# Optimization experiments

Hardware: AMD Instinct MI355X
Metric: run time of the kernel (lower is better)

Reference implementation:

```python
import jax, jax.numpy as jnp
import numpy as np

B, N, D, C = 64, 512, 1024, 4  # batch, num_electrodes, d_model, num_classes
H = D // 2


def setup_inputs() -> dict:
    key = jax.random.key(0)
    ks = jax.random.split(key, 16)
    s = 0.02
    return {
        "Q": jax.random.normal(ks[0], (B, N, D), jnp.float32),
        "K": jax.random.normal(ks[1], (B, N, D), jnp.float32),
        "V": jax.random.normal(ks[2], (B, N, D), jnp.float32),
        "electrode_ids": jnp.arange(N, dtype=jnp.int64 if jax.config.jax_enable_x64 else jnp.int32),
        "emb": jax.random.normal(ks[3], (N, D), jnp.float32) * s,
        "dw1": jax.random.normal(ks[4], (H, D), jnp.float32) * s,
        "db1": jnp.zeros((H,), jnp.float32),
        "dw2": jax.random.normal(ks[5], (1, H), jnp.float32) * s,
        "db2": jnp.zeros((1,), jnp.float32),
        "sw1": jax.random.normal(ks[6], (H, D), jnp.float32) * s,
        "sb1": jnp.zeros((H,), jnp.float32),
        "sw2": jax.random.normal(ks[7], (1, H), jnp.float32) * s,
        "sb2": jnp.zeros((1,), jnp.float32),
        "dopamine_scale": jnp.asarray(1.0, jnp.float32),
        "serotonin_scale": jnp.asarray(1.0, jnp.float32),
        "fc_w": jax.random.normal(ks[8], (C, N * D), jnp.float32) * s,
        "fc_b": jnp.zeros((C,), jnp.float32),
    }


def reference(Q, K, V, electrode_ids, emb, dw1, db1, dw2, db2,
              sw1, sb1, sw2, sb2, dopamine_scale, serotonin_scale, fc_w, fc_b):
    e = emb[electrode_ids]                       # [N, D]
    Q = Q + e
    K = K + e
    V = V + e
    scale = jnp.sqrt(jnp.asarray(D, jnp.float32))
    scores = jnp.einsum('bnd,bmd->bnm', Q, K) / scale          # [B, N, N]
    probs = jax.nn.softmax(scores, axis=-1)
    entropy = -jnp.sum(probs * jnp.log(probs + 1e-6), axis=-1)  # [B, N]

    # dopamine MLP on Q tokens (eval mode -> dropout is identity)
    dh = jax.nn.relu(jnp.einsum('bnd,hd->bnh', Q, dw1) + db1)
    dopamine = jax.nn.sigmoid(jnp.einsum('bnh,oh->bno', dh, dw2) + db2)[..., 0]  # [B, N]

    # serotonin MLP on entropy broadcast to D identical features:
    # Linear(entropy * ones(D)) == entropy * W1.sum(axis=1) + b1 (same math, no [B,N,D] temp)
    sh = jax.nn.relu(entropy[..., None] * jnp.sum(sw1, axis=1) + sb1)            # [B, N, H]
    serotonin = jax.nn.sigmoid(jnp.einsum('bnh,oh->bno', sh, sw2) + sb2)[..., 0]  # [B, N]

    mod = dopamine_scale * dopamine[..., None] - serotonin_scale * serotonin[..., None]
    ms = scores + mod
    mu = jnp.mean(ms, axis=-1, keepdims=True)
    sd = jnp.std(ms, axis=-1, keepdims=True, ddof=1)  # torch.std default is unbiased
    ms = (ms - mu) / (sd + 1e-6)
    probs2 = jax.nn.softmax(ms, axis=-1)
    attn_out = jnp.einsum('bnm,bmd->bnd', probs2, V)   # [B, N, D]
    flat = attn_out.reshape(attn_out.shape[0], -1)      # [B, N*D]
    return flat @ fc_w.T + fc_b                          # [B, C]
```

## Files before the change

kernel.cpp:

```cpp
#include <hip/hip_runtime.h>

#define NN 512
#define ND 1024
#define NDW 524288
#define NBATCH 64

typedef __attribute__((ext_vector_type(8))) __bf16 bf16x8;
typedef __attribute__((ext_vector_type(4))) float f32x4;
typedef unsigned short u16;
typedef unsigned int u32;

__device__ __forceinline__ u16 f2bf(float x) {
    u32 u = __float_as_uint(x);
    u = (u + 0x7fffu + ((u >> 16) & 1u)) >> 16;
    return (u16)u;
}
__device__ __forceinline__ float bf2f(u16 x) {
    return __uint_as_float(((u32)x) << 16);
}

union BF8 { bf16x8 v; u16 s[8]; };

__device__ __forceinline__ void dma16(const u16* g, const u16* l) {
    __builtin_amdgcn_global_load_lds(
        (const __attribute__((address_space(1))) u32*)(uintptr_t)g,
        (__attribute__((address_space(3))) u32*)(u32)(uintptr_t)l,
        16, 0, 0);
}

__global__ __launch_bounds__(256)
void nma_init_out(float* __restrict__ out, const float* __restrict__ fcb) {
    int t = threadIdx.x;
    if (t < NBATCH * 4) out[t] = fcb[t & 3];
}

__global__ __launch_bounds__(256)
void prep_ke(const float* __restrict__ K, const int* __restrict__ eid,
             const float* __restrict__ emb, u16* __restrict__ Ke) {
    size_t f = ((size_t)blockIdx.x * 256 + threadIdx.x) * 8;
    int n = (int)((f >> 10) & (NN - 1));
    int col = (int)(f & (ND - 1));
    const float* kp = K + f;
    const float* ep = emb + (size_t)eid[n] * ND + col;
    float4 k0 = *(const float4*)kp, k1 = *(const float4*)(kp + 4);
    float4 e0 = *(const float4*)ep, e1 = *(const float4*)(ep + 4);
    union { uint4 q; u16 s[8]; } o;
    o.s[0]=f2bf(k0.x+e0.x); o.s[1]=f2bf(k0.y+e0.y); o.s[2]=f2bf(k0.z+e0.z); o.s[3]=f2bf(k0.w+e0.w);
    o.s[4]=f2bf(k1.x+e1.x); o.s[5]=f2bf(k1.y+e1.y); o.s[6]=f2bf(k1.z+e1.z); o.s[7]=f2bf(k1.w+e1.w);
    *(uint4*)(Ke + f) = o.q;
}

__global__ __launch_bounds__(256)
void prep_vt(const float* __restrict__ V, const int* __restrict__ eid,
             const float* __restrict__ emb, u16* __restrict__ VT) {
    __shared__ u16 T[64 * 72];
    const int tid = threadIdx.x;
    const int b = blockIdx.z, d0 = blockIdx.y * 64, n0 = blockIdx.x * 64;
    {
        const int r = tid >> 2, cs = (tid & 3) * 16;
        const int n = n0 + r;
        const float* vp = V + ((size_t)b * NN + n) * ND + d0 + cs;
        const float* ep = emb + (size_t)eid[n] * ND + d0 + cs;
        #pragma unroll
        for (int j = 0; j < 4; ++j) {
            float4 v = *(const float4*)(vp + j * 4);
            float4 e = *(const float4*)(ep + j * 4);
            T[(cs + j*4 + 0) * 72 + r] = f2bf(v.x + e.x);
            T[(cs + j*4 + 1) * 72 + r] = f2bf(v.y + e.y);
            T[(cs + j*4 + 2) * 72 + r] = f2bf(v.z + e.z);
            T[(cs + j*4 + 3) * 72 + r] = f2bf(v.w + e.w);
        }
    }
    __syncthreads();
    {
        const int dr = tid >> 2, ms = (tid & 3) * 16;
        u16* dst = VT + ((size_t)b * ND + d0 + dr) * NN + n0 + ms;
        *(uint4*)dst       = *(const uint4*)&T[dr * 72 + ms];
        *(uint4*)(dst + 8) = *(const uint4*)&T[dr * 72 + ms + 8];
    }
}

__global__ __launch_bounds__(256, 2)
void nma_attn(const float* __restrict__ Q, const int* __restrict__ eid,
              const float* __restrict__ emb, const u16* __restrict__ Ke,
              const u16* __restrict__ VT, u16* __restrict__ O)
{
    __shared__ __align__(16) u16 KV[NN * 32];
    __shared__ __align__(16) u16 Ps[32 * 520];
    __shared__ float red[4][32][4];
    __shared__ float rowM[32], rowInv[32], rowRden[32];

    const int tid  = threadIdx.x;
    const int w    = tid >> 6;
    const int lane = tid & 63;
    const int q    = lane >> 4;
    const int l15  = lane & 15;
    const int bid  = blockIdx.x;
    const int jj   = bid >> 3;
    const int b    = (bid & 7) + ((jj >> 4) << 3);
    const int i0   = (jj & 15) * 32;
    const size_t bOff = (size_t)b * NN * ND;

    const float* Qrow0 = Q + bOff + (size_t)(i0 + l15) * ND;
    const float* Qrow1 = Q + bOff + (size_t)(i0 + 16 + l15) * ND;
    const float* Erow0 = emb + (size_t)eid[i0 + l15] * ND;
    const float* Erow1 = emb + (size_t)eid[i0 + 16 + l15] * ND;

    const u16* KeB = Ke + bOff;
    const u16* VTB = VT + (size_t)b * ND * NN;
    const int liw = w * 64 + lane;

    f32x4 acc[2][8];
    #pragma unroll
    for (int it = 0; it < 2; ++it)
        #pragma unroll
        for (int mt = 0; mt < 8; ++mt)
            acc[it][mt] = (f32x4){0.f, 0.f, 0.f, 0.f};

    for (int kc = 0; kc < 32; ++kc) {
        __syncthreads();
        #pragma unroll
        for (int ii = 0; ii < 8; ++ii) {
            const int li = ii * 256 + liw;
            const int m = li >> 2, seg = li & 3;
            dma16(KeB + (size_t)m * ND + kc * 32 + seg * 8,
                  &KV[(size_t)(ii * 256 + w * 64) * 8]);
        }
        BF8 a0u, a1u;
        {
            const int k0 = kc * 32 + q * 8;
            float4 x0 = *(const float4*)(Qrow0 + k0);
            float4 x1 = *(const float4*)(Qrow0 + k0 + 4);
            float4 e0 = *(const float4*)(Erow0 + k0);
            float4 e1 = *(const float4*)(Erow0 + k0 + 4);
            a0u.s[0] = f2bf(x0.x + e0.x); a0u.s[1] = f2bf(x0.y + e0.y);
            a0u.s[2] = f2bf(x0.z + e0.z); a0u.s[3] = f2bf(x0.w + e0.w);
            a0u.s[4] = f2bf(x1.x + e1.x); a0u.s[5] = f2bf(x1.y + e1.y);
            a0u.s[6] = f2bf(x1.z + e1.z); a0u.s[7] = f2bf(x1.w + e1.w);
            x0 = *(const float4*)(Qrow1 + k0);
            x1 = *(const float4*)(Qrow1 + k0 + 4);
            e0 = *(const float4*)(Erow1 + k0);
            e1 = *(const float4*)(Erow1 + k0 + 4);
            a1u.s[0] = f2bf(x0.x + e0.x); a1u.s[1] = f2bf(x0.y + e0.y);
            a1u.s[2] = f2bf(x0.z + e0.z); a1u.s[3] = f2bf(x0.w + e0.w);
            a1u.s[4] = f2bf(x1.x + e1.x); a1u.s[5] = f2bf(x1.y + e1.y);
            a1u.s[6] = f2bf(x1.z + e1.z); a1u.s[7] = f2bf(x1.w + e1.w);
        }
        __syncthreads();
        #pragma unroll
        for (int mt = 0; mt < 8; ++mt) {
            bf16x8 bf = *(const bf16x8*)&KV[(w * 128 + mt * 16 + l15) * 32 + q * 8];
            acc[0][mt] = __builtin_amdgcn_mfma_f32_16x16x32_bf16(a0u.v, bf, acc[0][mt], 0, 0, 0);
            acc[1][mt] = __builtin_amdgcn_mfma_f32_16x16x32_bf16(a1u.v, bf, acc[1][mt], 0, 0, 0);
        }
    }

    const float SC = 0.03125f;
    #pragma unroll
    for (int it = 0; it < 2; ++it)
        #pragma unroll
        for (int mt = 0; mt < 8; ++mt) {
            acc[it][mt][0] *= SC; acc[it][mt][1] *= SC;
            acc[it][mt][2] *= SC; acc[it][mt][3] *= SC;
        }
    float ssum[2][4], ssq[2][4], smax[2][4];
    #pragma unroll
    for (int it = 0; it < 2; ++it)
        #pragma unroll
        for (int r = 0; r < 4; ++r) {
            float s = 0.f, s2 = 0.f, mx = -3.4e38f;
            #pragma unroll
            for (int mt = 0; mt < 8; ++mt) {
                float v = acc[it][mt][r];
                s += v; s2 += v * v; mx = fmaxf(mx, v);
            }
            #pragma unroll
            for (int d = 1; d < 16; d <<= 1) {
                s  += __shfl_xor(s, d);
                s2 += __shfl_xor(s2, d);
                mx  = fmaxf(mx, __shfl_xor(mx, d));
            }
            ssum[it][r] = s; ssq[it][r] = s2; smax[it][r] = mx;
        }
    if (l15 == 0) {
        #pragma unroll
        for (int it = 0; it < 2; ++it)
            #pragma unroll
            for (int r = 0; r < 4; ++r) {
                int i = it * 16 + q * 4 + r;
                red[w][i][0] = ssum[it][r];
                red[w][i][1] = ssq[it][r];
                red[w][i][2] = smax[it][r];
            }
    }
    __syncthreads();
    if (tid < 32) {
        float s  = red[0][tid][0] + red[1][tid][0] + red[2][tid][0] + red[3][tid][0];
        float s2 = red[0][tid][1] + red[1][tid][1] + red[2][tid][1] + red[3][tid][1];
        float mx = fmaxf(fmaxf(red[0][tid][2], red[1][tid][2]),
                         fmaxf(red[2][tid][2], red[3][tid][2]));
        float mu  = s * (1.f / 512.f);
        float var = fmaxf((s2 - s * mu) * (1.f / 511.f), 0.f);
        float sd  = sqrtf(var);
        rowM[tid]   = mx;
        rowInv[tid] = 1.f / (sd + 1e-6f);
    }
    __syncthreads();
    float dsum[2][4];
    #pragma unroll
    for (int it = 0; it < 2; ++it)
        #pragma unroll
        for (int r = 0; r < 4; ++r) {
            int i = it * 16 + q * 4 + r;
            float M = rowM[i], inv = rowInv[i];
            float s = 0.f;
            #pragma unroll
            for (int mt = 0; mt < 8; ++mt) {
                float e = __expf((acc[it][mt][r] - M) * inv);
                acc[it][mt][r] = e; s += e;
            }
            #pragma unroll
            for (int d = 1; d < 16; d <<= 1) s += __shfl_xor(s, d);
            dsum[it][r] = s;
        }
    if (l15 == 0) {
        #pragma unroll
        for (int it = 0; it < 2; ++it)
            #pragma unroll
            for (int r = 0; r < 4; ++r)
                red[w][it * 16 + q * 4 + r][0] = dsum[it][r];
    }
    __syncthreads();
    if (tid < 32)
        rowRden[tid] = 1.f / (red[0][tid][0] + red[1][tid][0] + red[2][tid][0] + red[3][tid][0]);
    __syncthreads();
    #pragma unroll
    for (int it = 0; it < 2; ++it)
        #pragma unroll
        for (int r = 0; r < 4; ++r) {
            int i = it * 16 + q * 4 + r;
            float rd = rowRden[i];
            #pragma unroll
            for (int mt = 0; mt < 8; ++mt) {
                int m = w * 128 + mt * 16 + l15;
                Ps[i * 520 + m] = f2bf(acc[it][mt][r] * rd);
            }
        }

    for (int h = 0; h < 2; ++h) {
        f32x4 oacc[2][8];
        #pragma unroll
        for (int it = 0; it < 2; ++it)
            #pragma unroll
            for (int dt = 0; dt < 8; ++dt)
                oacc[it][dt] = (f32x4){0.f, 0.f, 0.f, 0.f};
        for (int mc = 0; mc < 16; ++mc) {
            __syncthreads();
            #pragma unroll
            for (int ii = 0; ii < 8; ++ii) {
                const int li = ii * 256 + liw;
                const int r = li >> 2, seg = li & 3;
                dma16(VTB + (size_t)(h * 512 + r) * NN + mc * 32 + seg * 8,
                      &KV[(size_t)(ii * 256 + w * 64) * 8]);
            }
            __syncthreads();
            bf16x8 p0 = *(const bf16x8*)&Ps[l15 * 520 + mc * 32 + q * 8];
            bf16x8 p1 = *(const bf16x8*)&Ps[(16 + l15) * 520 + mc * 32 + q * 8];
            #pragma unroll
            for (int dt = 0; dt < 8; ++dt) {
                bf16x8 bf = *(const bf16x8*)&KV[(w * 128 + dt * 16 + l15) * 32 + q * 8];
                oacc[0][dt] = __builtin_amdgcn_mfma_f32_16x16x32_bf16(p0, bf, oacc[0][dt], 0, 0, 0);
                oacc[1][dt] = __builtin_amdgcn_mfma_f32_16x16x32_bf16(p1, bf, oacc[1][dt], 0, 0, 0);
            }
        }
        #pragma unroll
        for (int it = 0; it < 2; ++it)
            #pragma unroll
            for (int dt = 0; dt < 8; ++dt) {
                const int dglob = h * 512 + w * 128 + dt * 16 + l15;
                #pragma unroll
                for (int r = 0; r < 4; ++r) {
                    const int iglob = i0 + it * 16 + q * 4 + r;
                    O[bOff + (size_t)iglob * ND + dglob] = f2bf(oacc[it][dt][r]);
                }
            }
    }
}

__global__ __launch_bounds__(256)
void fc_red(const u16* __restrict__ O, const float* __restrict__ fcw,
            float* __restrict__ out)
{
    __shared__ __align__(16) u16 Osh[64 * 264];
    __shared__ __align__(16) float Fsh[4 * 260];
    const int tid = threadIdx.x;
    const size_t nbase = (size_t)blockIdx.x * 1024;
    const int b = tid >> 2, c = tid & 3;
    float sum = 0.f;
    for (int ch = 0; ch < 4; ++ch) {
        __syncthreads();
        #pragma unroll
        for (int ii = 0; ii < 8; ++ii) {
            int si = ii * 256 + tid;
            int row = si >> 5, col8 = (si & 31) * 8;
            *(uint4*)&Osh[row * 264 + col8] =
                *(const uint4*)(O + (size_t)row * NDW + nbase + ch * 256 + col8);
        }
        {
            int cc = tid >> 6, n4 = (tid & 63) * 4;
            *(float4*)&Fsh[cc * 260 + n4] =
                *(const float4*)(fcw + (size_t)cc * NDW + nbase + ch * 256 + n4);
        }
        __syncthreads();
        #pragma unroll 4
        for (int n8 = 0; n8 < 32; ++n8) {
            union { uint4 v; u16 s[8]; } o4;
            o4.v = *(const uint4*)&Osh[b * 264 + n8 * 8];
            float4 f0 = *(const float4*)&Fsh[c * 260 + n8 * 8];
            float4 f1 = *(const float4*)&Fsh[c * 260 + n8 * 8 + 4];
            sum += bf2f(o4.s[0]) * f0.x + bf2f(o4.s[1]) * f0.y
                 + bf2f(o4.s[2]) * f0.z + bf2f(o4.s[3]) * f0.w
                 + bf2f(o4.s[4]) * f1.x + bf2f(o4.s[5]) * f1.y
                 + bf2f(o4.s[6]) * f1.z + bf2f(o4.s[7]) * f1.w;
        }
    }
    atomicAdd(&out[b * 4 + c], sum);
}

extern "C" void kernel_launch(void* const* d_in, const int* in_sizes, int n_in,
                              void* d_out, int out_size, void* d_ws, size_t ws_size,
                              hipStream_t stream) {
    (void)in_sizes; (void)n_in; (void)ws_size; (void)out_size;
    const float* Q   = (const float*)d_in[0];
    const float* K   = (const float*)d_in[1];
    const float* V   = (const float*)d_in[2];
    const int*   eid = (const int*)d_in[3];
    const float* emb = (const float*)d_in[4];
    const float* fcw = (const float*)d_in[15];
    const float* fcb = (const float*)d_in[16];
    float* out = (float*)d_out;

    u16* Ke = (u16*)d_ws;
    u16* VT = Ke + (size_t)NBATCH * NN * ND;
    u16* O  = VT + (size_t)NBATCH * NN * ND;

    nma_init_out<<<dim3(1), dim3(256), 0, stream>>>(out, fcb);
    prep_ke<<<dim3(16384), dim3(256), 0, stream>>>(K, eid, emb, Ke);
    prep_vt<<<dim3(8, 16, 64), dim3(256), 0, stream>>>(V, eid, emb, VT);
    nma_attn<<<dim3(1024), dim3(256), 0, stream>>>(Q, eid, emb, Ke, VT, O);
    fc_red<<<dim3(512), dim3(256), 0, stream>>>(O, fcw, out);
}
```

Measured before the change: 743.1 us.

## Make K/V tile DMA wave-private and software-pipeline loads to drop block barriers

The K and V^T tile DMA into LDS is remapped so each wave loads only the 128 rows it consumes itself. That removes the need for the two __syncthreads per k-chunk; explicit vmcnt/lgkmcnt waits are used instead. The next chunk's DMA is issued right after the current LDS fragments are read into registers, and the Q+emb global loads are double-buffered in registers. This overlaps memory traffic with MFMA work, at the cost of more registers and reliance on hand-tuned waitcnt ordering with global_load_lds.

```diff
diff --git a/kernel.cpp b/kernel.cpp
--- a/kernel.cpp
+++ b/kernel.cpp
@@ -95,20 +95,37 @@
     const int lane = tid & 63;
     const int q    = lane >> 4;
     const int l15  = lane & 15;
+    const int rr   = lane >> 2;
+    const int seg  = lane & 3;
     const int bid  = blockIdx.x;
     const int jj   = bid >> 3;
     const int b    = (bid & 7) + ((jj >> 4) << 3);
     const int i0   = (jj & 15) * 32;
     const size_t bOff = (size_t)b * NN * ND;
-
-    const float* Qrow0 = Q + bOff + (size_t)(i0 + l15) * ND;
-    const float* Qrow1 = Q + bOff + (size_t)(i0 + 16 + l15) * ND;
-    const float* Erow0 = emb + (size_t)eid[i0 + l15] * ND;
-    const float* Erow1 = emb + (size_t)eid[i0 + 16 + l15] * ND;
+    const int wrow = w * 128;
+
+    const float* Qr0 = Q + bOff + (size_t)(i0 + l15) * ND;
+    const float* Qr1 = Q + bOff + (size_t)(i0 + 16 + l15) * ND;
+    const float* Er0 = emb + (size_t)eid[i0 + l15] * ND;
+    const float* Er1 = emb + (size_t)eid[i0 + 16 + l15] * ND;
 
     const u16* KeB = Ke + bOff;
     const u16* VTB = VT + (size_t)b * ND * NN;
-    const int liw = w * 64 + lane;
+
+#define DMA_KE(KC) do {                                                         \
+    _Pragma("unroll")                                                           \
+    for (int ii_ = 0; ii_ < 8; ++ii_)                                           \
+        dma16(KeB + (size_t)(wrow + ii_ * 16 + rr) * ND + (KC) * 32 + seg * 8,  \
+              &KV[(wrow + ii_ * 16) * 32]);                                     \
+    } while (0)
+
+#define DMA_VT(H, MC) do {                                                      \
+    _Pragma("unroll")                                                           \
+    for (int ii_ = 0; ii_ < 8; ++ii_)                                           \
+        dma16(VTB + (size_t)((H) * 512 + wrow + ii_ * 16 + rr) * NN             \
+                  + (MC) * 32 + seg * 8,                                        \
+              &KV[(wrow + ii_ * 16) * 32]);                                     \
+    } while (0)
 
     f32x4 acc[2][8];
     #pragma unroll
@@ -117,42 +134,51 @@
         for (int mt = 0; mt < 8; ++mt)
             acc[it][mt] = (f32x4){0.f, 0.f, 0.f, 0.f};
 
-    for (int kc = 0; kc < 32; ++kc) {
-        __syncthreads();
-        #pragma unroll
-        for (int ii = 0; ii < 8; ++ii) {
-            const int li = ii * 256 + liw;
-            const int m = li >> 2, seg = li & 3;
-            dma16(KeB + (size_t)m * ND + kc * 32 + seg * 8,
-                  &KV[(size_t)(ii * 256 + w * 64) * 8]);
-        }
-        BF8 a0u, a1u;
-        {
-            const int k0 = kc * 32 + q * 8;
-            float4 x0 = *(const float4*)(Qrow0 + k0);
-            float4 x1 = *(const float4*)(Qrow0 + k0 + 4);
-            float4 e0 = *(const float4*)(Erow0 + k0);
-            float4 e1 = *(const float4*)(Erow0 + k0 + 4);
-            a0u.s[0] = f2bf(x0.x + e0.x); a0u.s[1] = f2bf(x0.y + e0.y);
-            a0u.s[2] = f2bf(x0.z + e0.z); a0u.s[3] = f2bf(x0.w + e0.w);
-            a0u.s[4] = f2bf(x1.x + e1.x); a0u.s[5] = f2bf(x1.y + e1.y);
-            a0u.s[6] = f2bf(x1.z + e1.z); a0u.s[7] = f2bf(x1.w + e1.w);
-            x0 = *(const float4*)(Qrow1 + k0);
-            x1 = *(const float4*)(Qrow1 + k0 + 4);
-            e0 = *(const float4*)(Erow1 + k0);
-            e1 = *(const float4*)(Erow1 + k0 + 4);
-            a1u.s[0] = f2bf(x0.x + e0.x); a1u.s[1] = f2bf(x0.y + e0.y);
-            a1u.s[2] = f2bf(x0.z + e0.z); a1u.s[3] = f2bf(x0.w + e0.w);
-            a1u.s[4] = f2bf(x1.x + e1.x); a1u.s[5] = f2bf(x1.y + e1.y);
-            a1u.s[6] = f2bf(x1.z + e1.z); a1u.s[7] = f2bf(x1.w + e1.w);
-        }
-        __syncthreads();
-        #pragma unroll
-        for (int mt = 0; mt < 8; ++mt) {
-            bf16x8 bf = *(const bf16x8*)&KV[(w * 128 + mt * 16 + l15) * 32 + q * 8];
-            acc[0][mt] = __builtin_amdgcn_mfma_f32_16x16x32_bf16(a0u.v, bf, acc[0][mt], 0, 0, 0);
-            acc[1][mt] = __builtin_amdgcn_mfma_f32_16x16x32_bf16(a1u.v, bf, acc[1][mt], 0, 0, 0);
-        }
+    float4 cur[8], nxt[8];
+    {
+        const int k0 = q * 8;
+        cur[0] = *(const float4*)(Qr0 + k0); cur[1] = *(const float4*)(Qr0 + k0 + 4);
+        cur[2] = *(const float4*)(Er0 + k0); cur[3] = *(const float4*)(Er0 + k0 + 4);
+        cur[4] = *(const float4*)(Qr1 + k0); cur[5] = *(const float4*)(Qr1 + k0 + 4);
+        cur[6] = *(const float4*)(Er1 + k0); cur[7] = *(const float4*)(Er1 + k0 + 4);
+        DMA_KE(0);
+    }
+
+#define P2BODY(KC, CUR, NXT) do {                                               \
+    BF8 a0u, a1u;                                                               \
+    a0u.s[0]=f2bf(CUR[0].x+CUR[2].x); a0u.s[1]=f2bf(CUR[0].y+CUR[2].y);         \
+    a0u.s[2]=f2bf(CUR[0].z+CUR[2].z); a0u.s[3]=f2bf(CUR[0].w+CUR[2].w);         \
+    a0u.s[4]=f2bf(CUR[1].x+CUR[3].x); a0u.s[5]=f2bf(CUR[1].y+CUR[3].y);         \
+    a0u.s[6]=f2bf(CUR[1].z+CUR[3].z); a0u.s[7]=f2bf(CUR[1].w+CUR[3].w);         \
+    a1u.s[0]=f2bf(CUR[4].x+CUR[6].x); a1u.s[1]=f2bf(CUR[4].y+CUR[6].y);         \
+    a1u.s[2]=f2bf(CUR[4].z+CUR[6].z); a1u.s[3]=f2bf(CUR[4].w+CUR[6].w);         \
+    a1u.s[4]=f2bf(CUR[5].x+CUR[7].x); a1u.s[5]=f2bf(CUR[5].y+CUR[7].y);         \
+    a1u.s[6]=f2bf(CUR[5].z+CUR[7].z); a1u.s[7]=f2bf(CUR[5].w+CUR[7].w);         \
+    if ((KC) < 31) {                                                            \
+        const int k0 = ((KC) + 1) * 32 + q * 8;                                 \
+        NXT[0] = *(const float4*)(Qr0 + k0); NXT[1] = *(const float4*)(Qr0 + k0 + 4); \
+        NXT[2] = *(const float4*)(Er0 + k0); NXT[3] = *(const float4*)(Er0 + k0 + 4); \
+        NXT[4] = *(const float4*)(Qr1 + k0); NXT[5] = *(const float4*)(Qr1 + k0 + 4); \
+        NXT[6] = *(const float4*)(Er1 + k0); NXT[7] = *(const float4*)(Er1 + k0 + 4); \
+        asm volatile("s_waitcnt vmcnt(8)" ::: "memory");      \
+    } else {                                                                    \
+        asm volatile("s_waitcnt vmcnt(0)" ::: "memory");                        \
+    }                                                                           \
+    bf16x8 bfr[8];                                                              \
+    _Pragma("unroll")                                                           \
+    for (int mt = 0; mt < 8; ++mt)                                              \
+        bfr[mt] = *(const bf16x8*)&KV[(wrow + mt * 16 + l15) * 32 + q * 8];     \
+    asm volatile("s_waitcnt lgkmcnt(0)" ::: "memory");          \
+    if ((KC) < 31) DMA_KE((KC) + 1);                     \
+    _Pragma("unroll")                                                           \
+    for (int mt = 0; mt < 8; ++mt) {                                            \
+        acc[0][mt] = __builtin_amdgcn_mfma_f32_16x16x32_bf16(a0u.v, bfr[mt], acc[0][mt], 0, 0, 0); \
+        acc[1][mt] = __builtin_amdgcn_mfma_f32_16x16x32_bf16(a1u.v, bfr[mt], acc[1][mt], 0, 0, 0); \
+    } } while (0)
+
+    for (int kc = 0; kc < 32; kc += 2) {
+        P2BODY(kc, cur, nxt);
+        P2BODY(kc + 1, nxt, cur);
     }
 
     const float SC = 0.03125f;
@@ -246,7 +272,9 @@
                 Ps[i * 520 + m] = f2bf(acc[it][mt][r] * rd);
             }
         }
-
+    __syncthreads();
+
+    DMA_VT(0, 0);
     for (int h = 0; h < 2; ++h) {
         f32x4 oacc[2][8];
         #pragma unroll
@@ -255,22 +283,23 @@
             for (int dt = 0; dt < 8; ++dt)
                 oacc[it][dt] = (f32x4){0.f, 0.f, 0.f, 0.f};
         for (int mc = 0; mc < 16; ++mc) {
-            __syncthreads();
-            #pragma unroll
-            for (int ii = 0; ii < 8; ++ii) {
-                const int li = ii * 256 + liw;
-                const int r = li >> 2, seg = li & 3;
-                dma16(VTB + (size_t)(h * 512 + r) * NN + mc * 32 + seg * 8,
-                      &KV[(size_t)(ii * 256 + w * 64) * 8]);
-            }
-            __syncthreads();
             bf16x8 p0 = *(const bf16x8*)&Ps[l15 * 520 + mc * 32 + q * 8];
             bf16x8 p1 = *(const bf16x8*)&Ps[(16 + l15) * 520 + mc * 32 + q * 8];
+            asm volatile("s_waitcnt vmcnt(0)" ::: "memory");
+            bf16x8 bfr[8];
+            #pragma unroll
+            for (int dt = 0; dt < 8; ++dt)
+                bfr[dt] = *(const bf16x8*)&KV[(wrow + dt * 16 + l15) * 32 + q * 8];
+            asm volatile("s_waitcnt lgkmcnt(0)" ::: "memory");
+            const int j = h * 16 + mc;
+            if (j < 31) {
+                const int jn = j + 1;
+                DMA_VT(jn >> 4, jn & 15);
+            }
             #pragma unroll
             for (int dt = 0; dt < 8; ++dt) {
-                bf16x8 bf = *(const bf16x8*)&KV[(w * 128 + dt * 16 + l15) * 32 + q * 8];
-                oacc[0][dt] = __builtin_amdgcn_mfma_f32_16x16x32_bf16(p0, bf, oacc[0][dt], 0, 0, 0);
-                oacc[1][dt] = __builtin_amdgcn_mfma_f32_16x16x32_bf16(p1, bf, oacc[1][dt], 0, 0, 0);
+                oacc[0][dt] = __builtin_amdgcn_mfma_f32_16x16x32_bf16(p0, bfr[dt], oacc[0][dt], 0, 0, 0);
+                oacc[1][dt] = __builtin_amdgcn_mfma_f32_16x16x32_bf16(p1, bfr[dt], oacc[1][dt], 0, 0, 0);
             }
         }
         #pragma unroll
@@ -285,6 +314,9 @@
                 }
             }
     }
+#undef P2BODY
+#undef DMA_KE
+#undef DMA_VT
 }
 
 __global__ __launch_bounds__(256)
```

After: 661.7 us. 10.9% less time.

## Fuse FC reduction into attention, drop LDS staging, precompute bf16 Q

Applied to the files above, without the earlier changes.

Q plus embedding is now converted to bf16 in the prep kernel alongside K. The attention kernel no longer stages K and V tiles in LDS; MFMA operands are read straight from global memory, which removes the per-chunk barriers and lets occupancy rise to 3 blocks per CU. The final FC projection is fused into the attention epilogue, so the bf16 O buffer and the separate fc_red kernel go away. In exchange, operand reuse now depends on L1/L2 instead of LDS, the fcw reads are strided, and the fused FC uses atomics per block.

```diff
diff --git a/kernel.cpp b/kernel.cpp
--- a/kernel.cpp
+++ b/kernel.cpp
@@ -15,18 +15,6 @@
     u = (u + 0x7fffu + ((u >> 16) & 1u)) >> 16;
     return (u16)u;
 }
-__device__ __forceinline__ float bf2f(u16 x) {
-    return __uint_as_float(((u32)x) << 16);
-}
-
-union BF8 { bf16x8 v; u16 s[8]; };
-
-__device__ __forceinline__ void dma16(const u16* g, const u16* l) {
-    __builtin_amdgcn_global_load_lds(
-        (const __attribute__((address_space(1))) u32*)(uintptr_t)g,
-        (__attribute__((address_space(3))) u32*)(u32)(uintptr_t)l,
-        16, 0, 0);
-}
 
 __global__ __launch_bounds__(256)
 void nma_init_out(float* __restrict__ out, const float* __restrict__ fcb) {
@@ -35,19 +23,30 @@
 }
 
 __global__ __launch_bounds__(256)
-void prep_ke(const float* __restrict__ K, const int* __restrict__ eid,
-             const float* __restrict__ emb, u16* __restrict__ Ke) {
+void prep_qk(const float* __restrict__ Q, const float* __restrict__ K,
+             const int* __restrict__ eid, const float* __restrict__ emb,
+             u16* __restrict__ Qe, u16* __restrict__ Ke) {
     size_t f = ((size_t)blockIdx.x * 256 + threadIdx.x) * 8;
     int n = (int)((f >> 10) & (NN - 1));
     int col = (int)(f & (ND - 1));
-    const float* kp = K + f;
     const float* ep = emb + (size_t)eid[n] * ND + col;
-    float4 k0 = *(const float4*)kp, k1 = *(const float4*)(kp + 4);
     float4 e0 = *(const float4*)ep, e1 = *(const float4*)(ep + 4);
-    union { uint4 q; u16 s[8]; } o;
-    o.s[0]=f2bf(k0.x+e0.x); o.s[1]=f2bf(k0.y+e0.y); o.s[2]=f2bf(k0.z+e0.z); o.s[3]=f2bf(k0.w+e0.w);
-    o.s[4]=f2bf(k1.x+e1.x); o.s[5]=f2bf(k1.y+e1.y); o.s[6]=f2bf(k1.z+e1.z); o.s[7]=f2bf(k1.w+e1.w);
-    *(uint4*)(Ke + f) = o.q;
+    {
+        const float* qp = Q + f;
+        float4 x0 = *(const float4*)qp, x1 = *(const float4*)(qp + 4);
+        union { uint4 u; u16 s[8]; } o;
+        o.s[0]=f2bf(x0.x+e0.x); o.s[1]=f2bf(x0.y+e0.y); o.s[2]=f2bf(x0.z+e0.z); o.s[3]=f2bf(x0.w+e0.w);
+        o.s[4]=f2bf(x1.x+e1.x); o.s[5]=f2bf(x1.y+e1.y); o.s[6]=f2bf(x1.z+e1.z); o.s[7]=f2bf(x1.w+e1.w);
+        *(uint4*)(Qe + f) = o.u;
+    }
+    {
+        const float* kp = K + f;
+        float4 x0 = *(const float4*)kp, x1 = *(const float4*)(kp + 4);
+        union { uint4 u; u16 s[8]; } o;
+        o.s[0]=f2bf(x0.x+e0.x); o.s[1]=f2bf(x0.y+e0.y); o.s[2]=f2bf(x0.z+e0.z); o.s[3]=f2bf(x0.w+e0.w);
+        o.s[4]=f2bf(x1.x+e1.x); o.s[5]=f2bf(x1.y+e1.y); o.s[6]=f2bf(x1.z+e1.z); o.s[7]=f2bf(x1.w+e1.w);
+        *(uint4*)(Ke + f) = o.u;
+    }
 }
 
 __global__ __launch_bounds__(256)
@@ -80,12 +79,11 @@
     }
 }
 
-__global__ __launch_bounds__(256, 2)
-void nma_attn(const float* __restrict__ Q, const int* __restrict__ eid,
-              const float* __restrict__ emb, const u16* __restrict__ Ke,
-              const u16* __restrict__ VT, u16* __restrict__ O)
+__global__ __launch_bounds__(256, 3)
+void nma_attn(const u16* __restrict__ Qe, const u16* __restrict__ Ke,
+              const u16* __restrict__ VT, const float* __restrict__ fcw,
+              float* __restrict__ out)
 {
-    __shared__ __align__(16) u16 KV[NN * 32];
     __shared__ __align__(16) u16 Ps[32 * 520];
     __shared__ float red[4][32][4];
     __shared__ float rowM[32], rowInv[32], rowRden[32];
@@ -100,15 +98,7 @@
     const int b    = (bid & 7) + ((jj >> 4) << 3);
     const int i0   = (jj & 15) * 32;
     const size_t bOff = (size_t)b * NN * ND;
-
-    const float* Qrow0 = Q + bOff + (size_t)(i0 + l15) * ND;
-    const float* Qrow1 = Q + bOff + (size_t)(i0 + 16 + l15) * ND;
-    const float* Erow0 = emb + (size_t)eid[i0 + l15] * ND;
-    const float* Erow1 = emb + (size_t)eid[i0 + 16 + l15] * ND;
-
-    const u16* KeB = Ke + bOff;
-    const u16* VTB = VT + (size_t)b * ND * NN;
-    const int liw = w * 64 + lane;
+    const int wrow = w * 128;
 
     f32x4 acc[2][8];
     #pragma unroll
@@ -117,41 +107,20 @@
         for (int mt = 0; mt < 8; ++mt)
             acc[it][mt] = (f32x4){0.f, 0.f, 0.f, 0.f};
 
-    for (int kc = 0; kc < 32; ++kc) {
-        __syncthreads();
-        #pragma unroll
-        for (int ii = 0; ii < 8; ++ii) {
-            const int li = ii * 256 + liw;
-            const int m = li >> 2, seg = li & 3;
-            dma16(KeB + (size_t)m * ND + kc * 32 + seg * 8,
-                  &KV[(size_t)(ii * 256 + w * 64) * 8]);
-        }
-        BF8 a0u, a1u;
-        {
-            const int k0 = kc * 32 + q * 8;
-            float4 x0 = *(const float4*)(Qrow0 + k0);
-            float4 x1 = *(const float4*)(Qrow0 + k0 + 4);
-            float4 e0 = *(const float4*)(Erow0 + k0);
-            float4 e1 = *(const float4*)(Erow0 + k0 + 4);
-            a0u.s[0] = f2bf(x0.x + e0.x); a0u.s[1] = f2bf(x0.y + e0.y);
-            a0u.s[2] = f2bf(x0.z + e0.z); a0u.s[3] = f2bf(x0.w + e0.w);
-            a0u.s[4] = f2bf(x1.x + e1.x); a0u.s[5] = f2bf(x1.y + e1.y);
-            a0u.s[6] = f2bf(x1.z + e1.z); a0u.s[7] = f2bf(x1.w + e1.w);
-            x0 = *(const float4*)(Qrow1 + k0);
-            x1 = *(const float4*)(Qrow1 + k0 + 4);
-            e0 = *(const float4*)(Erow1 + k0);
-            e1 = *(const float4*)(Erow1 + k0 + 4);
-            a1u.s[0] = f2bf(x0.x + e0.x); a1u.s[1] = f2bf(x0.y + e0.y);
-            a1u.s[2] = f2bf(x0.z + e0.z); a1u.s[3] = f2bf(x0.w + e0.w);
-            a1u.s[4] = f2bf(x1.x + e1.x); a1u.s[5] = f2bf(x1.y + e1.y);
-            a1u.s[6] = f2bf(x1.z + e1.z); a1u.s[7] = f2bf(x1.w + e1.w);
-        }
-        __syncthreads();
-        #pragma unroll
-        for (int mt = 0; mt < 8; ++mt) {
-            bf16x8 bf = *(const bf16x8*)&KV[(w * 128 + mt * 16 + l15) * 32 + q * 8];
-            acc[0][mt] = __builtin_amdgcn_mfma_f32_16x16x32_bf16(a0u.v, bf, acc[0][mt], 0, 0, 0);
-            acc[1][mt] = __builtin_amdgcn_mfma_f32_16x16x32_bf16(a1u.v, bf, acc[1][mt], 0, 0, 0);
+    {
+        const u16* aP0 = Qe + bOff + (size_t)(i0 + l15) * ND + q * 8;
+        const u16* aP1 = aP0 + (size_t)16 * ND;
+        const u16* bP  = Ke + bOff + (size_t)(wrow + l15) * ND + q * 8;
+        for (int kc = 0; kc < 32; ++kc) {
+            const int ko = kc * 32;
+            bf16x8 a0 = *(const bf16x8*)(aP0 + ko);
+            bf16x8 a1 = *(const bf16x8*)(aP1 + ko);
+            #pragma unroll
+            for (int mt = 0; mt < 8; ++mt) {
+                bf16x8 bf = *(const bf16x8*)(bP + (size_t)(mt * 16) * ND + ko);
+                acc[0][mt] = __builtin_amdgcn_mfma_f32_16x16x32_bf16(a0, bf, acc[0][mt], 0, 0, 0);
+                acc[1][mt] = __builtin_amdgcn_mfma_f32_16x16x32_bf16(a1, bf, acc[1][mt], 0, 0, 0);
+            }
         }
     }
 
@@ -246,7 +215,9 @@
                 Ps[i * 520 + m] = f2bf(acc[it][mt][r] * rd);
             }
         }
-
+    __syncthreads();
+
+    float fsum[4] = {0.f, 0.f, 0.f, 0.f};
     for (int h = 0; h < 2; ++h) {
         f32x4 oacc[2][8];
         #pragma unroll
@@ -254,77 +225,50 @@
             #pragma unroll
             for (int dt = 0; dt < 8; ++dt)
                 oacc[it][dt] = (f32x4){0.f, 0.f, 0.f, 0.f};
+        const u16* vP = VT + (size_t)b * ND * NN
+                      + (size_t)(h * 512 + wrow + l15) * NN + q * 8;
         for (int mc = 0; mc < 16; ++mc) {
-            __syncthreads();
-            #pragma unroll
-            for (int ii = 0; ii < 8; ++ii) {
-                const int li = ii * 256 + liw;
-                const int r = li >> 2, seg = li & 3;
-                dma16(VTB + (size_t)(h * 512 + r) * NN + mc * 32 + seg * 8,
-                      &KV[(size_t)(ii * 256 + w * 64) * 8]);
-            }
-            __syncthreads();
             bf16x8 p0 = *(const bf16x8*)&Ps[l15 * 520 + mc * 32 + q * 8];
             bf16x8 p1 = *(const bf16x8*)&Ps[(16 + l15) * 520 + mc * 32 + q * 8];
             #pragma unroll
             for (int dt = 0; dt < 8; ++dt) {
-                bf16x8 bf = *(const bf16x8*)&KV[(w * 128 + dt * 16 + l15) * 32 + q * 8];
+                bf16x8 bf = *(const bf16x8*)(vP + (size_t)(dt * 16) * NN + mc * 32);
                 oacc[0][dt] = __builtin_amdgcn_mfma_f32_16x16x32_bf16(p0, bf, oacc[0][dt], 0, 0, 0);
                 oacc[1][dt] = __builtin_amdgcn_mfma_f32_16x16x32_bf16(p1, bf, oacc[1][dt], 0, 0, 0);
             }
         }
         #pragma unroll
-        for (int it = 0; it < 2; ++it)
-            #pragma unroll
-            for (int dt = 0; dt < 8; ++dt) {
-                const int dglob = h * 512 + w * 128 + dt * 16 + l15;
+        for (int it = 0; it < 2; ++it) {
+            #pragma unroll
+            for (int r = 0; r < 4; ++r) {
+                const int iglob = i0 + it * 16 + q * 4 + r;
+                const float* fr = fcw + (size_t)iglob * ND + (h * 512 + wrow + l15);
                 #pragma unroll
-                for (int r = 0; r < 4; ++r) {
-                    const int iglob = i0 + it * 16 + q * 4 + r;
-                    O[bOff + (size_t)iglob * ND + dglob] = f2bf(oacc[it][dt][r]);
+                for (int dt = 0; dt < 8; ++dt) {
+                    float o = oacc[0][dt][r];
+                    if (it == 1) o = oacc[1][dt][r];
+                    fsum[0] += o * fr[dt * 16];
+                    fsum[1] += o * fr[(size_t)NDW + dt * 16];
+                    fsum[2] += o * fr[(size_t)2 * NDW + dt * 16];
+                    fsum[3] += o * fr[(size_t)3 * NDW + dt * 16];
                 }
             }
-    }
-}
-
-__global__ __launch_bounds__(256)
-void fc_red(const u16* __restrict__ O, const float* __restrict__ fcw,
-            float* __restrict__ out)
-{
-    __shared__ __align__(16) u16 Osh[64 * 264];
-    __shared__ __align__(16) float Fsh[4 * 260];
-    const int tid = threadIdx.x;
-    const size_t nbase = (size_t)blockIdx.x * 1024;
-    const int b = tid >> 2, c = tid & 3;
-    float sum = 0.f;
-    for (int ch = 0; ch < 4; ++ch) {
-        __syncthreads();
-        #pragma unroll
-        for (int ii = 0; ii < 8; ++ii) {
-            int si = ii * 256 + tid;
-            int row = si >> 5, col8 = (si & 31) * 8;
-            *(uint4*)&Osh[row * 264 + col8] =
-                *(const uint4*)(O + (size_t)row * NDW + nbase + ch * 256 + col8);
-        }
-        {
-            int cc = tid >> 6, n4 = (tid & 63) * 4;
-            *(float4*)&Fsh[cc * 260 + n4] =
-                *(const float4*)(fcw + (size_t)cc * NDW + nbase + ch * 256 + n4);
-        }
-        __syncthreads();
-        #pragma unroll 4
-        for (int n8 = 0; n8 < 32; ++n8) {
-            union { uint4 v; u16 s[8]; } o4;
-            o4.v = *(const uint4*)&Osh[b * 264 + n8 * 8];
-            float4 f0 = *(const float4*)&Fsh[c * 260 + n8 * 8];
-            float4 f1 = *(const float4*)&Fsh[c * 260 + n8 * 8 + 4];
-            sum += bf2f(o4.s[0]) * f0.x + bf2f(o4.s[1]) * f0.y
-                 + bf2f(o4.s[2]) * f0.z + bf2f(o4.s[3]) * f0.w
-                 + bf2f(o4.s[4]) * f1.x + bf2f(o4.s[5]) * f1.y
-                 + bf2f(o4.s[6]) * f1.z + bf2f(o4.s[7]) * f1.w;
-        }
-    }
-    atomicAdd(&out[b * 4 + c], sum);
+        }
+    }
+    #pragma unroll
+    for (int c = 0; c < 4; ++c)
+        #pragma unroll
+        for (int d = 1; d < 64; d <<= 1)
+            fsum[c] += __shfl_xor(fsum[c], d);
+    if (lane == 0) {
+        red[w][0][0] = fsum[0]; red[w][0][1] = fsum[1];
+        red[w][0][2] = fsum[2]; red[w][0][3] = fsum[3];
+    }
+    __syncthreads();
+    if (tid < 4) {
+        float s = red[0][0][tid] + red[1][0][tid] + red[2][0][tid] + red[3][0][tid];
+        atomicAdd(&out[b * 4 + tid], s);
+    }
 }
 
 extern "C" void kernel_launch(void* const* d_in, const int* in_sizes, int n_in,
@@ -340,13 +284,12 @@
     const float* fcb = (const float*)d_in[16];
     float* out = (float*)d_out;
 
-    u16* Ke = (u16*)d_ws;
+    u16* Qe = (u16*)d_ws;
+    u16* Ke = Qe + (size_t)NBATCH * NN * ND;
     u16* VT = Ke + (size_t)NBATCH * NN * ND;
-    u16* O  = VT + (size_t)NBATCH * NN * ND;
 
     nma_init_out<<<dim3(1), dim3(256), 0, stream>>>(out, fcb);
-    prep_ke<<<dim3(16384), dim3(256), 0, stream>>>(K, eid, emb, Ke);
+    prep_qk<<<dim3(16384), dim3(256), 0, stream>>>(Q, K, eid, emb, Qe, Ke);
     prep_vt<<<dim3(8, 16, 64), dim3(256), 0, stream>>>(V, eid, emb, VT);
-    nma_attn<<<dim3(1024), dim3(256), 0, stream>>>(Q, eid, emb, Ke, VT, O);
-    fc_red<<<dim3(512), dim3(256), 0, stream>>>(O, fcw, out);
-}
+    nma_attn<<<dim3(1024), dim3(256), 0, stream>>>(Qe, Ke, VT, fcw, out);
+}
```

After: 801.4 us. 1.08x slower.
